# Kernel tuning notes

Measured on AMD Instinct MI355X. Metric: run time of the kernel, lower is better.

The kernel has to match this reference:

```python
import jax, jax.numpy as jnp
import numpy as np

T, B, I, H = 2048, 64, 256, 256


def setup_inputs() -> dict:
    key = jax.random.key(0)
    ks = jax.random.split(key, 7)
    s = 1.0 / np.sqrt(H)  # torch LSTMCell init scale
    return {
        "input": jax.random.normal(ks[0], (T, B, I), dtype=jnp.float32),
        "h0": jax.random.normal(ks[1], (B, H), dtype=jnp.float32),
        "c0": jax.random.normal(ks[2], (B, H), dtype=jnp.float32),
        "W_ih": jax.random.uniform(ks[3], (4 * H, I), jnp.float32, -s, s),
        "W_hh": jax.random.uniform(ks[4], (4 * H, H), jnp.float32, -s, s),
        "b_ih": jax.random.uniform(ks[5], (4 * H,), jnp.float32, -s, s),
        "b_hh": jax.random.uniform(ks[6], (4 * H,), jnp.float32, -s, s),
    }


def reference(input, h0, c0, W_ih, W_hh, b_ih, b_hh):
    # Precompute the input contribution for all timesteps in one big GEMM:
    # [T,B,I] @ [I,4H] -> [T,B,4H]
    x_gates = jnp.einsum("tbi,gi->tbg", input, W_ih) + b_ih + b_hh

    def step(carry, xg):
        h, c = carry
        gates = xg + h @ W_hh.T  # [B,4H]
        i, f, g, o = jnp.split(gates, 4, axis=-1)  # torch gate order i,f,g,o
        i = jax.nn.sigmoid(i)
        f = jax.nn.sigmoid(f)
        g = jnp.tanh(g)
        o = jax.nn.sigmoid(o)
        c_new = f * c + i * g
        h_new = o * jnp.tanh(c_new)
        return (h_new, c_new), h_new

    (h_T, c_T), outputs = jax.lax.scan(step, (h0, c0), x_gates)
    return outputs, (h_T, c_T)
```

## Files before the change

kernel.cpp:

```cpp
#include <hip/hip_runtime.h>


#define TT 2048
#define BB 64
#define HH 256
#define GG 1024

#define EXCH_OFF 0
#define CST_OFF 0x40000
#define XG_OFF 0x50000

#define BM 128
#define BN 128
#define BK 64
#define LDT 132

__device__ __forceinline__ float sigm(float x) { return 1.0f / (1.0f + __expf(-x)); }
__device__ __forceinline__ float tanh_(float x) {
  float e = __expf(2.0f * x);
  return 1.0f - 2.0f / (e + 1.0f);
}

__global__ __launch_bounds__(256, 2) void lstm_xgates(
    const float* __restrict__ xin,
    const float* __restrict__ Wih,
    const float* __restrict__ bih, const float* __restrict__ bhh,
    float* __restrict__ xg,
    int t0, int ct)
{
  const int rows = ct * BB;
  const int tid = (int)threadIdx.x;
  const int mb = (int)blockIdx.x >> 3;
  const int cb = (int)blockIdx.x & 7;
  const int row0 = mb * BM;
  const int col0 = cb * BN;

  __shared__ __align__(16) float As[BK][LDT];
  __shared__ __align__(16) float Bs[BK][LDT];

  const int sc = tid & 15;
  const int sr = tid >> 4;
  const int tm = tid >> 4;
  const int tn = tid & 15;

  const float* xbase = xin + (size_t)t0 * BB * HH;

  float4 xa[8], wb[8];
#pragma unroll
  for (int i = 0; i < 8; ++i) {
    int gr = row0 + sr + 16 * i;
    int grc = gr < rows ? gr : 0;
    xa[i] = *(const float4*)(xbase + (size_t)grc * HH + 4 * sc);
    wb[i] = *(const float4*)(Wih + (size_t)(col0 + sr + 16 * i) * HH + 4 * sc);
  }

  float acc[8][8];
#pragma unroll
  for (int i = 0; i < 8; ++i)
#pragma unroll
    for (int j = 0; j < 8; ++j) acc[i][j] = 0.f;

  const int KT = HH / BK;
  for (int kt = 0; kt < KT; ++kt) {
#pragma unroll
    for (int i = 0; i < 8; ++i) {
      int r = sr + 16 * i;
      As[4 * sc + 0][r] = xa[i].x;
      As[4 * sc + 1][r] = xa[i].y;
      As[4 * sc + 2][r] = xa[i].z;
      As[4 * sc + 3][r] = xa[i].w;
      Bs[4 * sc + 0][r] = wb[i].x;
      Bs[4 * sc + 1][r] = wb[i].y;
      Bs[4 * sc + 2][r] = wb[i].z;
      Bs[4 * sc + 3][r] = wb[i].w;
    }
    __syncthreads();

    if (kt + 1 < KT) {
      const int k0 = (kt + 1) * BK;
#pragma unroll
      for (int i = 0; i < 8; ++i) {
        int gr = row0 + sr + 16 * i;
        int grc = gr < rows ? gr : 0;
        xa[i] = *(const float4*)(xbase + (size_t)grc * HH + k0 + 4 * sc);
        wb[i] = *(const float4*)(Wih + (size_t)(col0 + sr + 16 * i) * HH + k0 + 4 * sc);
      }
    }

#pragma unroll 4
    for (int k = 0; k < BK; ++k) {
      float4 a0 = *(const float4*)(&As[k][8 * tm]);
      float4 a1 = *(const float4*)(&As[k][8 * tm + 4]);
      float4 b0 = *(const float4*)(&Bs[k][4 * tn]);
      float4 b1 = *(const float4*)(&Bs[k][64 + 4 * tn]);
      const float av[8] = {a0.x, a0.y, a0.z, a0.w, a1.x, a1.y, a1.z, a1.w};
      const float bv[8] = {b0.x, b0.y, b0.z, b0.w, b1.x, b1.y, b1.z, b1.w};
#pragma unroll
      for (int i = 0; i < 8; ++i)
#pragma unroll
        for (int j = 0; j < 8; ++j)
          acc[i][j] = fmaf(av[i], bv[j], acc[i][j]);
    }
    __syncthreads();
  }

  const float4 bi0 = *(const float4*)(bih + col0 + 4 * tn);
  const float4 bh0 = *(const float4*)(bhh + col0 + 4 * tn);
  const float4 bi1 = *(const float4*)(bih + col0 + 64 + 4 * tn);
  const float4 bh1 = *(const float4*)(bhh + col0 + 64 + 4 * tn);
  const float4 bia0 = make_float4(bi0.x + bh0.x, bi0.y + bh0.y, bi0.z + bh0.z, bi0.w + bh0.w);
  const float4 bia1 = make_float4(bi1.x + bh1.x, bi1.y + bh1.y, bi1.z + bh1.z, bi1.w + bh1.w);

#pragma unroll
  for (int i = 0; i < 8; ++i) {
    int r = row0 + 8 * tm + i;
    if (r < rows) {
      float4 o0 = make_float4(acc[i][0] + bia0.x, acc[i][1] + bia0.y,
                              acc[i][2] + bia0.z, acc[i][3] + bia0.w);
      float4 o1 = make_float4(acc[i][4] + bia1.x, acc[i][5] + bia1.y,
                              acc[i][6] + bia1.z, acc[i][7] + bia1.w);
      float* op = xg + (size_t)r * GG + col0;
      *(float4*)(op + 4 * tn) = o0;
      *(float4*)(op + 64 + 4 * tn) = o1;
    }
  }
}

__global__ __launch_bounds__(512, 2) void lstm_rec(
    const float* __restrict__ h0, const float* __restrict__ c0,
    const float* __restrict__ Whh,
    const float* __restrict__ xg,
    float* __restrict__ out,
    unsigned long long* exch,
    float* __restrict__ cstate,
    int t0, int t1)
{
  const int tid = threadIdx.x;
  const int wblk = blockIdx.x;
  const int r = wblk & 7, q = (wblk >> 3) & 3, s5 = wblk >> 5;
  const int b = 8 * s5 + r;

  const int rl = tid >> 1;
  const int hf = tid & 1;
  const int g = rl >> 6;
  const int u = rl & 63;
  const int grow = 256 * g + 64 * q + u;

  float wvf[128];
  {
    const float4* wp = (const float4*)(Whh + (size_t)grow * HH);
#pragma unroll
    for (int k = 0; k < 32; ++k) {
      float4 w = wp[2 * k + hf];
      wvf[4 * k + 0] = w.x;
      wvf[4 * k + 1] = w.y;
      wvf[4 * k + 2] = w.z;
      wvf[4 * k + 3] = w.w;
    }
#pragma unroll
    for (int k = 0; k < 32; ++k)
      asm volatile("" : "+v"(wvf[4 * k + 0]), "+v"(wvf[4 * k + 1]),
                        "+v"(wvf[4 * k + 2]), "+v"(wvf[4 * k + 3]));
  }

  float cst = 0.f;
  if (tid < 64) {
    const int jj = 64 * q + tid;
    cst = (t0 == 0) ? c0[b * HH + jj] : cstate[b * HH + jj];
  }

  __shared__ __align__(16) float hbf[256];
  __shared__ float gl[256];

  unsigned long long* exb = exch + b * 512;
  const int sidx = (tid + 64 * q) & 255;

  float xgv = __builtin_nontemporal_load(xg + (size_t)b * GG + grow);
  float xgn1 = 0.f;
  if (t0 + 1 < t1)
    xgn1 = __builtin_nontemporal_load(xg + ((size_t)BB + b) * GG + grow);

  for (int t = t0; t < t1; ++t) {
    if (t == 0) {
      if (tid < 256) hbf[sidx] = h0[b * HH + sidx];
    } else if (t == t0 || (tid >= 64 && tid < 256)) {
      if (tid < 256) {
        unsigned long long* slot = exb + ((t & 1) << 8) + sidx;
        unsigned long long wd;
        do {
          wd = __hip_atomic_load(slot, __ATOMIC_RELAXED, __HIP_MEMORY_SCOPE_AGENT);
        } while ((unsigned int)(wd >> 32) != (unsigned int)t);
        union { unsigned int i; float f; } cv;
        cv.i = (unsigned int)wd;
        hbf[sidx] = cv.f;
      }
    }
    __syncthreads();

    float xgn2 = 0.f;
    if (t + 2 < t1)
      xgn2 = __builtin_nontemporal_load(
          xg + ((size_t)(t + 2 - t0) * BB + b) * GG + grow);

    float a0 = hf ? 0.f : xgv, a1 = 0.f, a2 = 0.f, a3 = 0.f;
    {
      const float4* hq = (const float4*)hbf;
#pragma unroll
      for (int k = 0; k < 32; ++k) {
        float4 hv4 = hq[2 * k + hf];
        a0 = fmaf(wvf[4 * k + 0], hv4.x, a0);
        a1 = fmaf(wvf[4 * k + 1], hv4.y, a1);
        a2 = fmaf(wvf[4 * k + 2], hv4.z, a2);
        a3 = fmaf(wvf[4 * k + 3], hv4.w, a3);
      }
    }
    float s = (a0 + a1) + (a2 + a3);
    s += __shfl_xor(s, 1);
    if (!hf) gl[rl] = s;
    xgv = xgn1;
    xgn1 = xgn2;
    __syncthreads();

    if (tid < 64) {
      const float gi = gl[tid];
      const float gf = gl[64 + tid];
      const float gg = gl[128 + tid];
      const float go = gl[192 + tid];
      const float ig = sigm(gi), fg = sigm(gf), gc = tanh_(gg), og = sigm(go);
      cst = fg * cst + ig * gc;
      const float hv = og * tanh_(cst);
      const int jj = 64 * q + tid;
      union { float f; unsigned int i; } hu;
      hu.f = hv;
      __hip_atomic_exchange(exb + (((t + 1) & 1) << 8) + jj,
                            (((unsigned long long)(unsigned int)(t + 1)) << 32) | hu.i,
                            __ATOMIC_RELAXED, __HIP_MEMORY_SCOPE_AGENT);
      hbf[jj] = hv;
      __builtin_nontemporal_store(hv, &out[(size_t)t * (BB * HH) + (size_t)b * HH + jj]);
      if (t == TT - 1) {
        const size_t base = (size_t)TT * (BB * HH);
        out[base + (size_t)b * HH + jj] = hv;
        out[base + BB * HH + (size_t)b * HH + jj] = cst;
      }
      if (t == t1 - 1) cstate[b * HH + jj] = cst;
    }
  }
}

extern "C" void kernel_launch(void* const* d_in, const int* in_sizes, int n_in,
                              void* d_out, int out_size, void* d_ws, size_t ws_size,
                              hipStream_t stream) {
  const float* xin = (const float*)d_in[0];
  const float* h0 = (const float*)d_in[1];
  const float* c0 = (const float*)d_in[2];
  const float* Wih = (const float*)d_in[3];
  const float* Whh = (const float*)d_in[4];
  const float* bih = (const float*)d_in[5];
  const float* bhh = (const float*)d_in[6];
  float* out = (float*)d_out;

  char* ws = (char*)d_ws;
  unsigned long long* exch = (unsigned long long*)(ws + EXCH_OFF);
  float* cstate = (float*)(ws + CST_OFF);
  float* xg = (float*)(ws + XG_OFF);

  size_t avail = (ws_size > XG_OFF) ? (ws_size - XG_OFF) : 0;
  long chunkT = (long)(avail / ((size_t)BB * GG * sizeof(float)));
  if (chunkT > TT) chunkT = TT;
  if (chunkT < 1) chunkT = 1;

  hipMemsetAsync(ws + EXCH_OFF, 0, 0x40000, stream);
  for (int t0 = 0; t0 < TT; t0 += (int)chunkT) {
    int ct = (TT - t0 < chunkT) ? (TT - t0) : (int)chunkT;
    int mblk = (ct * BB + BM - 1) / BM;
    hipLaunchKernelGGL(lstm_xgates, dim3(mblk * (GG / BN)), dim3(256), 0, stream,
                       xin, Wih, bih, bhh, xg, t0, ct);
    hipLaunchKernelGGL(lstm_rec, dim3(256), dim3(512), 0, stream,
                       h0, c0, Whh, xg, out, exch, cstate, t0, t0 + ct);
  }
}
```

Baseline: 5.398 ms.

## Split recurrent matvec across 16 lanes per four gate rows with 1024-thread blocks

The recurrent kernel now runs 1024 threads per block. Each group of 16 lanes computes four gate rows, each lane covering a 16-element slice of K, with a butterfly shuffle reduction. Register-held weights per thread drop from 128 to 64 floats, which shortens each thread's serial FMA chain per step and makes more warps available to hide latency. The cost is extra shuffle reduction steps, one block per CU, and float4 xg loads that now go only through lanes with kc==0.

```diff
diff --git a/kernel.cpp b/kernel.cpp
--- a/kernel.cpp
+++ b/kernel.cpp
@@ -126,7 +126,7 @@
   }
 }
 
-__global__ __launch_bounds__(512, 2) void lstm_rec(
+__global__ __launch_bounds__(1024, 1) void lstm_rec(
     const float* __restrict__ h0, const float* __restrict__ c0,
     const float* __restrict__ Whh,
     const float* __restrict__ xg,
@@ -140,25 +140,27 @@
   const int r = wblk & 7, q = (wblk >> 3) & 3, s5 = wblk >> 5;
   const int b = 8 * s5 + r;
 
-  const int rl = tid >> 1;
-  const int hf = tid & 1;
-  const int g = rl >> 6;
-  const int u = rl & 63;
-  const int grow = 256 * g + 64 * q + u;
-
-  float wvf[128];
+  const int rg = tid >> 4;
+  const int kc = tid & 15;
+  const int g = rg >> 4;
+  const int grow0 = 256 * g + 64 * q + 4 * (rg & 15);
+
+  float wvf[64];
   {
-    const float4* wp = (const float4*)(Whh + (size_t)grow * HH);
-#pragma unroll
-    for (int k = 0; k < 32; ++k) {
-      float4 w = wp[2 * k + hf];
-      wvf[4 * k + 0] = w.x;
-      wvf[4 * k + 1] = w.y;
-      wvf[4 * k + 2] = w.z;
-      wvf[4 * k + 3] = w.w;
-    }
-#pragma unroll
-    for (int k = 0; k < 32; ++k)
+#pragma unroll
+    for (int rr = 0; rr < 4; ++rr) {
+      const float4* wp = (const float4*)(Whh + (size_t)(grow0 + rr) * HH);
+#pragma unroll
+      for (int j = 0; j < 4; ++j) {
+        float4 w = wp[kc + 16 * j];
+        wvf[16 * rr + 4 * j + 0] = w.x;
+        wvf[16 * rr + 4 * j + 1] = w.y;
+        wvf[16 * rr + 4 * j + 2] = w.z;
+        wvf[16 * rr + 4 * j + 3] = w.w;
+      }
+    }
+#pragma unroll
+    for (int k = 0; k < 16; ++k)
       asm volatile("" : "+v"(wvf[4 * k + 0]), "+v"(wvf[4 * k + 1]),
                         "+v"(wvf[4 * k + 2]), "+v"(wvf[4 * k + 3]));
   }
@@ -170,15 +172,18 @@
   }
 
   __shared__ __align__(16) float hbf[256];
-  __shared__ float gl[256];
+  __shared__ __align__(16) float gl[256];
 
   unsigned long long* exb = exch + b * 512;
   const int sidx = (tid + 64 * q) & 255;
 
-  float xgv = __builtin_nontemporal_load(xg + (size_t)b * GG + grow);
-  float xgn1 = 0.f;
-  if (t0 + 1 < t1)
-    xgn1 = __builtin_nontemporal_load(xg + ((size_t)BB + b) * GG + grow);
+  const bool xgl = (kc == 0);
+  float4 xgv = make_float4(0.f, 0.f, 0.f, 0.f), xgn1 = xgv;
+  if (xgl) {
+    xgv = *(const float4*)(xg + (size_t)b * GG + grow0);
+    if (t0 + 1 < t1)
+      xgn1 = *(const float4*)(xg + ((size_t)BB + b) * GG + grow0);
+  }
 
   for (int t = t0; t < t1; ++t) {
     if (t == 0) {
@@ -197,26 +202,45 @@
     }
     __syncthreads();
 
-    float xgn2 = 0.f;
-    if (t + 2 < t1)
-      xgn2 = __builtin_nontemporal_load(
-          xg + ((size_t)(t + 2 - t0) * BB + b) * GG + grow);
-
-    float a0 = hf ? 0.f : xgv, a1 = 0.f, a2 = 0.f, a3 = 0.f;
+    float4 xgn2 = make_float4(0.f, 0.f, 0.f, 0.f);
+    if (xgl && t + 2 < t1)
+      xgn2 = *(const float4*)(xg + ((size_t)(t + 2 - t0) * BB + b) * GG + grow0);
+
+    float ac0 = 0.f, ac1 = 0.f, ac2 = 0.f, ac3 = 0.f;
     {
       const float4* hq = (const float4*)hbf;
 #pragma unroll
-      for (int k = 0; k < 32; ++k) {
-        float4 hv4 = hq[2 * k + hf];
-        a0 = fmaf(wvf[4 * k + 0], hv4.x, a0);
-        a1 = fmaf(wvf[4 * k + 1], hv4.y, a1);
-        a2 = fmaf(wvf[4 * k + 2], hv4.z, a2);
-        a3 = fmaf(wvf[4 * k + 3], hv4.w, a3);
-      }
-    }
-    float s = (a0 + a1) + (a2 + a3);
-    s += __shfl_xor(s, 1);
-    if (!hf) gl[rl] = s;
+      for (int j = 0; j < 4; ++j) {
+        float4 h4 = hq[kc + 16 * j];
+        ac0 = fmaf(wvf[4 * j + 0], h4.x, ac0);
+        ac0 = fmaf(wvf[4 * j + 1], h4.y, ac0);
+        ac0 = fmaf(wvf[4 * j + 2], h4.z, ac0);
+        ac0 = fmaf(wvf[4 * j + 3], h4.w, ac0);
+        ac1 = fmaf(wvf[16 + 4 * j + 0], h4.x, ac1);
+        ac1 = fmaf(wvf[16 + 4 * j + 1], h4.y, ac1);
+        ac1 = fmaf(wvf[16 + 4 * j + 2], h4.z, ac1);
+        ac1 = fmaf(wvf[16 + 4 * j + 3], h4.w, ac1);
+        ac2 = fmaf(wvf[32 + 4 * j + 0], h4.x, ac2);
+        ac2 = fmaf(wvf[32 + 4 * j + 1], h4.y, ac2);
+        ac2 = fmaf(wvf[32 + 4 * j + 2], h4.z, ac2);
+        ac2 = fmaf(wvf[32 + 4 * j + 3], h4.w, ac2);
+        ac3 = fmaf(wvf[48 + 4 * j + 0], h4.x, ac3);
+        ac3 = fmaf(wvf[48 + 4 * j + 1], h4.y, ac3);
+        ac3 = fmaf(wvf[48 + 4 * j + 2], h4.z, ac3);
+        ac3 = fmaf(wvf[48 + 4 * j + 3], h4.w, ac3);
+      }
+    }
+#pragma unroll
+    for (int m = 1; m < 16; m <<= 1) {
+      ac0 += __shfl_xor(ac0, m);
+      ac1 += __shfl_xor(ac1, m);
+      ac2 += __shfl_xor(ac2, m);
+      ac3 += __shfl_xor(ac3, m);
+    }
+    if (xgl) {
+      float4 o = make_float4(ac0 + xgv.x, ac1 + xgv.y, ac2 + xgv.z, ac3 + xgv.w);
+      *(float4*)(&gl[4 * rg]) = o;
+    }
     xgv = xgn1;
     xgn1 = xgn2;
     __syncthreads();
@@ -275,7 +299,7 @@
     int mblk = (ct * BB + BM - 1) / BM;
     hipLaunchKernelGGL(lstm_xgates, dim3(mblk * (GG / BN)), dim3(256), 0, stream,
                        xin, Wih, bih, bhh, xg, t0, ct);
-    hipLaunchKernelGGL(lstm_rec, dim3(256), dim3(512), 0, stream,
+    hipLaunchKernelGGL(lstm_rec, dim3(256), dim3(1024), 0, stream,
                        h0, c0, Whh, xg, out, exch, cstate, t0, t0 + ct);
   }
 }
```

New measurement: 4.998 ms. -7.4%, faster.
